# Performance work log

Hardware: AMD Instinct MI355X
Metric: run time of the kernel (lower is better)

The kernel has to match this reference:

```python
import jax, jax.numpy as jnp
import numpy as np

# Static problem sizes (see shape_source)
B, SX, SY = 256, 256, 70          # graphs, encoder nodes/graph, decoder nodes/graph
F, EMB, H = 512, 256, 256          # f_size, emb_size, h_size
VOCAB = 256
E = 4 * B * SY                     # 71680 edges
N_SLT = 4                          # SltEdgeTypes
N_SRT = 8                          # len(SrtEdgeTypes)


def setup_inputs() -> dict:
    key = jax.random.key(0)
    ks = jax.random.split(key, 24)
    s = 0.02
    inp = {
        'x': jax.random.normal(ks[0], (B * SX, F), jnp.float32),
        'x_batch': jnp.repeat(jnp.arange(B, dtype=jnp.int64), SX),
        'tgt_y': jax.random.randint(ks[1], (B * SY,), 0, VOCAB, jnp.int64),
        'tgt_edge_index': jax.random.randint(ks[2], (2, E), 0, B * SY, jnp.int64),
        'tgt_edge_type': jax.random.randint(ks[3], (E,), 0, N_SLT, jnp.int64),
        'tgt_y_batch': jnp.repeat(jnp.arange(B, dtype=jnp.int64), SY),
        'embeds': jax.random.normal(ks[4], (VOCAB, EMB), jnp.float32) * s,
    }
    dims = [(EMB, H), (H, H), (H, EMB)]
    k = 5
    for l, (din, dout) in enumerate(dims, start=1):
        inp[f'W_in{l}'] = jax.random.normal(ks[k + 0], (din, dout), jnp.float32) * s
        inp[f'Wq{l}'] = jax.random.normal(ks[k + 1], (dout, F), jnp.float32) * s
        inp[f'Wv{l}'] = jax.random.normal(ks[k + 2], (F, dout), jnp.float32) * s
        inp[f'Ee{l}'] = jax.random.normal(ks[k + 3], (N_SLT, dout), jnp.float32) * s
        k += 4
    inp['lin_z_w'] = jax.random.normal(ks[k], (EMB, VOCAB), jnp.float32) * s
    inp['lin_z_b'] = jnp.zeros((VOCAB,), jnp.float32)
    inp['lin_g_w'] = jax.random.normal(ks[k + 1], (2 * EMB, N_SRT), jnp.float32) * s
    inp['lin_g_b'] = jnp.zeros((N_SRT,), jnp.float32)
    return inp


def gcn_dec_layer(x_b, y, src, tgt, etype, W_in, Wq, Wv, Ee):
    """Edge-type-conditioned message passing + cross-attention onto encoder x.
    x_b: [B,SX,F]; y: [Ny,din]. Returns ([Ny,dout], alpha [B,SY,SX])."""
    h = y @ W_in                                   # [Ny, dout]
    m = h[src] + Ee[etype]                         # gather + type embedding
    agg = jax.ops.segment_sum(m, tgt, num_segments=y.shape[0])
    q = (h @ Wq).reshape(B, SY, F)                 # query into encoder space
    logits = jnp.einsum('bqf,bkf->bqk', q, x_b) / jnp.sqrt(jnp.float32(F))
    alpha = jax.nn.softmax(logits, axis=-1)        # [B,SY,SX]
    ctx = jnp.einsum('bqk,bkf->bqf', alpha, x_b) @ Wv  # [B,SY,dout]
    out = jax.nn.relu(h + agg + ctx.reshape(h.shape[0], -1))
    return out, alpha


def reference(x, x_batch, tgt_y, tgt_edge_index, tgt_edge_type, tgt_y_batch,
              embeds, W_in1, Wq1, Wv1, Ee1, W_in2, Wq2, Wv2, Ee2,
              W_in3, Wq3, Wv3, Ee3, lin_z_w, lin_z_b, lin_g_w, lin_g_b):
    x_b = x.reshape(B, SX, F)
    src, tgt = tgt_edge_index[0], tgt_edge_index[1]
    y = embeds[tgt_y]                              # [Ny, EMB]
    y, a1 = gcn_dec_layer(x_b, y, src, tgt, tgt_edge_type, W_in1, Wq1, Wv1, Ee1)
    y, a2 = gcn_dec_layer(x_b, y, src, tgt, tgt_edge_type, W_in2, Wq2, Wv2, Ee2)
    y, a3 = gcn_dec_layer(x_b, y, src, tgt, tgt_edge_type, W_in3, Wq3, Wv3, Ee3)
    y_score = y @ lin_z_w + lin_z_b                # [Ny, VOCAB]
    ef = y[tgt_edge_index]                         # [2, E, EMB]
    ef = jnp.transpose(ef, (1, 0, 2)).reshape(E, 2 * EMB)
    y_edge_rel_score = ef @ lin_g_w + lin_g_b      # [E, N_SRT]
    return (y, y_score, y_edge_rel_score, a1, a2, a3)
```

## Files before the change

### kernel.cpp

```cpp
#include <hip/hip_runtime.h>
#include <cstddef>
#include <cstdint>

#define B_    256
#define SX_   256
#define SY_   70
#define F_    512
#define EMB_  256
#define NY_   (B_*SY_)
#define NE_   (4*B_*SY_)

typedef short s16x8 __attribute__((ext_vector_type(8)));
typedef float f32x4 __attribute__((ext_vector_type(4)));
typedef unsigned short us4 __attribute__((ext_vector_type(4)));
typedef unsigned short us8 __attribute__((ext_vector_type(8)));

__device__ __forceinline__ unsigned short f2bf(float f) {
    unsigned u = __builtin_bit_cast(unsigned, f);
    u += 0x7fffu + ((u >> 16) & 1u);
    return (unsigned short)(u >> 16);
}
__device__ __forceinline__ float bf2f(unsigned short b) {
    unsigned u = ((unsigned)b) << 16;
    return __builtin_bit_cast(float, u);
}

template<int EPI>
__global__ __launch_bounds__(256, 2)
void gemm_mfma(const unsigned short* __restrict__ A, int lda, long sAb,
               const unsigned short* __restrict__ Bt, int ldb, long sBb,
               float* __restrict__ Cf, int ldc, long sCfb,
               unsigned short* __restrict__ Cb, int ldcb, long sCbb,
               const float* __restrict__ aux1, long sAux,
               int M, int K, float scale)
{
    __shared__ unsigned short As[128 * 64];
    __shared__ unsigned short Bs[128 * 64];
    char* AsB = (char*)As;
    char* BsB = (char*)Bs;
    const int tid = threadIdx.x;
    const int z = blockIdx.z;
    A  += (size_t)z * sAb;
    Bt += (size_t)z * sBb;
    if (aux1) aux1 += (size_t)z * sAux;
    const int bm = blockIdx.y * 128, bn = blockIdx.x * 128;
    const int lane = tid & 63;
    const int w = tid >> 6, wr = w >> 1, wc = w & 1;
    const int l15 = lane & 15, lq = lane >> 4;

    f32x4 acc[4][4];
    const f32x4 z4 = {0.f, 0.f, 0.f, 0.f};
#pragma unroll
    for (int m = 0; m < 4; ++m)
#pragma unroll
        for (int n = 0; n < 4; ++n) acc[m][n] = z4;

    for (int k0 = 0; k0 < K; k0 += 64) {
#pragma unroll
        for (int i = 0; i < 4; ++i) {
            const int row = i * 32 + (tid >> 3);
            const int k8  = (tid & 7) ^ (row & 7);
            int ra = bm + row; ra = (ra < M) ? ra : (M - 1);
            const unsigned short* g = A + (size_t)ra * lda + k0 + k8 * 8;
            __builtin_amdgcn_global_load_lds(
                (const __attribute__((address_space(1))) unsigned int*)g,
                (__attribute__((address_space(3))) unsigned int*)(AsB + i * 4096 + tid * 16),
                16, 0, 0);
        }
#pragma unroll
        for (int i = 0; i < 4; ++i) {
            const int row = i * 32 + (tid >> 3);
            const int k8  = (tid & 7) ^ (row & 7);
            const unsigned short* g = Bt + (size_t)(bn + row) * ldb + k0 + k8 * 8;
            __builtin_amdgcn_global_load_lds(
                (const __attribute__((address_space(1))) unsigned int*)g,
                (__attribute__((address_space(3))) unsigned int*)(BsB + i * 4096 + tid * 16),
                16, 0, 0);
        }
        __syncthreads();
#pragma unroll
        for (int kk = 0; kk < 2; ++kk) {
            s16x8 af[4], bf[4];
#pragma unroll
            for (int m = 0; m < 4; ++m) {
                const int row = wr * 64 + m * 16 + l15;
                const int slot = (kk * 4 + lq) ^ (row & 7);
                af[m] = *(const s16x8*)(AsB + row * 128 + slot * 16);
            }
#pragma unroll
            for (int n = 0; n < 4; ++n) {
                const int col = wc * 64 + n * 16 + l15;
                const int slot = (kk * 4 + lq) ^ (col & 7);
                bf[n] = *(const s16x8*)(BsB + col * 128 + slot * 16);
            }
#pragma unroll
            for (int m = 0; m < 4; ++m)
#pragma unroll
                for (int n = 0; n < 4; ++n)
                    acc[m][n] = __builtin_amdgcn_mfma_f32_16x16x32_bf16(
                        af[m], bf[n], acc[m][n], 0, 0, 0);
        }
        __syncthreads();
    }

    float* cf = Cf ? Cf + (size_t)z * sCfb : nullptr;
    unsigned short* cb = Cb ? Cb + (size_t)z * sCbb : nullptr;
#pragma unroll
    for (int m = 0; m < 4; ++m) {
#pragma unroll
        for (int n = 0; n < 4; ++n) {
            const int col = bn + wc * 64 + n * 16 + l15;
            f32x4 v = acc[m][n];
#pragma unroll
            for (int r = 0; r < 4; ++r) {
                const int gr = bm + wr * 64 + m * 16 + lq * 4 + r;
                if (gr >= M) continue;
                float o = v[r] * scale;
                if (EPI == 4) o += aux1[col];
                if (EPI == 5) {
                    o += aux1[(size_t)gr * ldc + col];
                    o = fmaxf(o, 0.f);
                }
                if (cf) cf[(size_t)gr * ldc + col] = o;
                if (cb) cb[(size_t)gr * ldcb + col] = f2bf(o);
            }
        }
    }
}

__global__ __launch_bounds__(256, 1)
void attn_logits_sm(const unsigned short* __restrict__ Q,
                    const unsigned short* __restrict__ X,
                    float* __restrict__ Aout,
                    unsigned short* __restrict__ Ab,
                    float scale)
{
    __shared__ unsigned short As[128 * 64];
    __shared__ unsigned short Bs[256 * 64];
    __shared__ float red[2][2][64];
    char* AsB = (char*)As;
    char* BsB = (char*)Bs;
    const int tid = threadIdx.x;
    const int z = blockIdx.x;
    const unsigned short* Qb = Q + (size_t)z * SY_ * F_;
    const unsigned short* Xb = X + (size_t)z * SX_ * F_;
    const int lane = tid & 63;
    const int w = tid >> 6, wr = w >> 1, wc = w & 1;
    const int l15 = lane & 15, lq = lane >> 4;

    f32x4 acc[4][8];
    const f32x4 z4 = {0.f, 0.f, 0.f, 0.f};
#pragma unroll
    for (int m = 0; m < 4; ++m)
#pragma unroll
        for (int n = 0; n < 8; ++n) acc[m][n] = z4;

    for (int k0 = 0; k0 < F_; k0 += 64) {
#pragma unroll
        for (int i = 0; i < 4; ++i) {
            const int row = i * 32 + (tid >> 3);
            const int k8  = (tid & 7) ^ (row & 7);
            const int ra = (row < SY_) ? row : (SY_ - 1);
            const unsigned short* g = Qb + (size_t)ra * F_ + k0 + k8 * 8;
            __builtin_amdgcn_global_load_lds(
                (const __attribute__((address_space(1))) unsigned int*)g,
                (__attribute__((address_space(3))) unsigned int*)(AsB + i * 4096 + tid * 16),
                16, 0, 0);
        }
#pragma unroll
        for (int i = 0; i < 8; ++i) {
            const int row = i * 32 + (tid >> 3);
            const int k8  = (tid & 7) ^ (row & 7);
            const unsigned short* g = Xb + (size_t)row * F_ + k0 + k8 * 8;
            __builtin_amdgcn_global_load_lds(
                (const __attribute__((address_space(1))) unsigned int*)g,
                (__attribute__((address_space(3))) unsigned int*)(BsB + i * 4096 + tid * 16),
                16, 0, 0);
        }
        __syncthreads();
#pragma unroll
        for (int kk = 0; kk < 2; ++kk) {
            s16x8 af[4], bf[8];
#pragma unroll
            for (int m = 0; m < 4; ++m) {
                const int row = wr * 64 + m * 16 + l15;
                const int slot = (kk * 4 + lq) ^ (row & 7);
                af[m] = *(const s16x8*)(AsB + row * 128 + slot * 16);
            }
#pragma unroll
            for (int n = 0; n < 8; ++n) {
                const int col = wc * 128 + n * 16 + l15;
                const int slot = (kk * 4 + lq) ^ (col & 7);
                bf[n] = *(const s16x8*)(BsB + col * 128 + slot * 16);
            }
#pragma unroll
            for (int m = 0; m < 4; ++m)
#pragma unroll
                for (int n = 0; n < 8; ++n)
                    acc[m][n] = __builtin_amdgcn_mfma_f32_16x16x32_bf16(
                        af[m], bf[n], acc[m][n], 0, 0, 0);
        }
        __syncthreads();
    }

#pragma unroll
    for (int m = 0; m < 4; ++m)
#pragma unroll
        for (int n = 0; n < 8; ++n)
#pragma unroll
            for (int r = 0; r < 4; ++r) acc[m][n][r] *= scale;

    float rmax[4][4];
#pragma unroll
    for (int m = 0; m < 4; ++m)
#pragma unroll
        for (int r = 0; r < 4; ++r) {
            float mx = acc[m][0][r];
#pragma unroll
            for (int n = 1; n < 8; ++n) mx = fmaxf(mx, acc[m][n][r]);
            mx = fmaxf(mx, __shfl_xor(mx, 1));
            mx = fmaxf(mx, __shfl_xor(mx, 2));
            mx = fmaxf(mx, __shfl_xor(mx, 4));
            mx = fmaxf(mx, __shfl_xor(mx, 8));
            rmax[m][r] = mx;
        }
    if (l15 == 0) {
#pragma unroll
        for (int m = 0; m < 4; ++m)
#pragma unroll
            for (int r = 0; r < 4; ++r)
                red[wc][wr][m * 16 + lq * 4 + r] = rmax[m][r];
    }
    __syncthreads();
    float rtot[4][4];
#pragma unroll
    for (int m = 0; m < 4; ++m)
#pragma unroll
        for (int r = 0; r < 4; ++r) {
            const int lr = m * 16 + lq * 4 + r;
            rtot[m][r] = fmaxf(red[0][wr][lr], red[1][wr][lr]);
        }
    __syncthreads();
    float rsum[4][4];
#pragma unroll
    for (int m = 0; m < 4; ++m)
#pragma unroll
        for (int r = 0; r < 4; ++r) {
            float s = 0.f;
#pragma unroll
            for (int n = 0; n < 8; ++n) {
                float e = __expf(acc[m][n][r] - rtot[m][r]);
                acc[m][n][r] = e;
                s += e;
            }
            s += __shfl_xor(s, 1);
            s += __shfl_xor(s, 2);
            s += __shfl_xor(s, 4);
            s += __shfl_xor(s, 8);
            rsum[m][r] = s;
        }
    if (l15 == 0) {
#pragma unroll
        for (int m = 0; m < 4; ++m)
#pragma unroll
            for (int r = 0; r < 4; ++r)
                red[wc][wr][m * 16 + lq * 4 + r] = rsum[m][r];
    }
    __syncthreads();
    float* ao = Aout + (size_t)z * SY_ * SX_;
    unsigned short* ab = Ab + (size_t)z * SY_ * SX_;
#pragma unroll
    for (int m = 0; m < 4; ++m)
#pragma unroll
        for (int r = 0; r < 4; ++r) {
            const int lr = m * 16 + lq * 4 + r;
            const int row = wr * 64 + lr;
            if (row >= SY_) continue;
            const float inv = 1.0f / (red[0][wr][lr] + red[1][wr][lr]);
#pragma unroll
            for (int n = 0; n < 8; ++n) {
                const int col = wc * 128 + n * 16 + l15;
                const float o = acc[m][n][r] * inv;
                ao[(size_t)row * SX_ + col] = o;
                ab[(size_t)row * SX_ + col] = f2bf(o);
            }
        }
}

__global__ __launch_bounds__(256)
void conv_x(const float* __restrict__ in, unsigned short* __restrict__ out, int n8)
{
    for (int i = blockIdx.x * 256 + threadIdx.x; i < n8; i += 2048 * 256) {
        float4 a = ((const float4*)in)[i * 2];
        float4 b = ((const float4*)in)[i * 2 + 1];
        us8 o = { f2bf(a.x), f2bf(a.y), f2bf(a.z), f2bf(a.w),
                  f2bf(b.x), f2bf(b.y), f2bf(b.z), f2bf(b.w) };
        ((us8*)out)[i] = o;
    }
}

struct WAll {
    const float* src[10];
    unsigned short* dst[10];
    int R[10];
    int C[10];
};

__global__ __launch_bounds__(256)
void conv_wT_all(WAll d)
{
    const int z = blockIdx.z;
    const int R = d.R[z], C = d.C[z];
    const int c0 = blockIdx.x * 64, r0 = blockIdx.y * 64;
    if (c0 >= C || r0 >= R) return;
    const float* in = d.src[z];
    unsigned short* outT = d.dst[z];
    __shared__ unsigned short t[64][65];
    const int r = threadIdx.x >> 4, cq = (threadIdx.x & 15) << 2;
#pragma unroll
    for (int i = 0; i < 4; ++i) {
        const int rr = r + i * 16;
        float4 v = *(const float4*)(in + (size_t)(r0 + rr) * C + c0 + cq);
        t[rr][cq + 0] = f2bf(v.x); t[rr][cq + 1] = f2bf(v.y);
        t[rr][cq + 2] = f2bf(v.z); t[rr][cq + 3] = f2bf(v.w);
    }
    __syncthreads();
    const int c = threadIdx.x >> 2, sq = (threadIdx.x & 3) << 4;
    us8 o0, o1;
#pragma unroll
    for (int i = 0; i < 8; ++i) { o0[i] = t[sq + i][c]; o1[i] = t[sq + 8 + i][c]; }
    *(us8*)(outT + (size_t)(c0 + c) * R + r0 + sq) = o0;
    *(us8*)(outT + (size_t)(c0 + c) * R + r0 + sq + 8) = o1;
}

__global__ __launch_bounds__(256)
void gather_embed(const float* __restrict__ embeds, const int* __restrict__ tgt_y,
                  unsigned short* __restrict__ yb)
{
    const int i = blockIdx.x * 8 + (threadIdx.x >> 5);
    const int c8 = (threadIdx.x & 31) * 8;
    const int v = tgt_y[i];
    const float* p = embeds + (size_t)v * 256 + c8;
    float4 a = *(const float4*)p;
    float4 b = *(const float4*)(p + 4);
    us8 o = { f2bf(a.x), f2bf(a.y), f2bf(a.z), f2bf(a.w),
              f2bf(b.x), f2bf(b.y), f2bf(b.z), f2bf(b.w) };
    *(us8*)(yb + (size_t)i * 256 + c8) = o;
}

__global__ __launch_bounds__(256)
void edge_deg(const int* __restrict__ tgt, int* __restrict__ deg)
{
    const int e = blockIdx.x * 256 + threadIdx.x;
    if (e < NE_) atomicAdd(&deg[tgt[e]], 1);
}

__global__ __launch_bounds__(1024)
void scan_off(const int* __restrict__ deg, int* __restrict__ off, int* __restrict__ cursor)
{
    __shared__ int ls[1024];
    const int t = threadIdx.x;
    const int base = t * 18;
    int local[18];
    int s = 0;
#pragma unroll
    for (int i = 0; i < 18; ++i) {
        const int idx = base + i;
        const int v = (idx < NY_) ? deg[idx] : 0;
        local[i] = s; s += v;
    }
    ls[t] = s;
    __syncthreads();
    for (int d = 1; d < 1024; d <<= 1) {
        int v = (t >= d) ? ls[t - d] : 0;
        __syncthreads();
        ls[t] += v;
        __syncthreads();
    }
    const int excl = (t == 0) ? 0 : ls[t - 1];
#pragma unroll
    for (int i = 0; i < 18; ++i) {
        const int idx = base + i;
        if (idx < NY_) {
            const int o = excl + local[i];
            off[idx] = o; cursor[idx] = o;
        }
    }
    if (t == 1023) off[NY_] = ls[1023];
}

__global__ __launch_bounds__(256)
void edge_fill(const int* __restrict__ tgt, int* __restrict__ cursor,
               int* __restrict__ elist)
{
    const int e = blockIdx.x * 256 + threadIdx.x;
    if (e >= NE_) return;
    const int pos = atomicAdd(&cursor[tgt[e]], 1);
    elist[pos] = e;
}

__global__ __launch_bounds__(256)
void node_agg(const unsigned short* __restrict__ hb,
              const float* __restrict__ Ee,
              const int* __restrict__ src, const int* __restrict__ etype,
              const int* __restrict__ off, const int* __restrict__ elist,
              float* __restrict__ agg)
{
    const int nid  = blockIdx.x * 4 + (threadIdx.x >> 6);
    const int lane = threadIdx.x & 63;
    const int c = lane * 4;
    const int k0 = off[nid], k1 = off[nid + 1];
    us4 sv = *(const us4*)(hb + (size_t)nid * 256 + c);
    float4 acc;
    acc.x = bf2f(sv[0]); acc.y = bf2f(sv[1]);
    acc.z = bf2f(sv[2]); acc.w = bf2f(sv[3]);
    int cnt0 = 0, cnt1 = 0, cnt2 = 0, cnt3 = 0;
    for (int k = k0; k < k1; ++k) {
        const int e = elist[k];
        const int sfrom = src[e];
        const int ty = etype[e];
        us4 hv = *(const us4*)(hb + (size_t)sfrom * 256 + c);
        acc.x += bf2f(hv[0]); acc.y += bf2f(hv[1]);
        acc.z += bf2f(hv[2]); acc.w += bf2f(hv[3]);
        cnt0 += (ty == 0); cnt1 += (ty == 1); cnt2 += (ty == 2); cnt3 += (ty == 3);
    }
    float4 e0 = *(const float4*)(Ee + c);
    float4 e1 = *(const float4*)(Ee + 256 + c);
    float4 e2 = *(const float4*)(Ee + 512 + c);
    float4 e3 = *(const float4*)(Ee + 768 + c);
    acc.x += cnt0 * e0.x + cnt1 * e1.x + cnt2 * e2.x + cnt3 * e3.x;
    acc.y += cnt0 * e0.y + cnt1 * e1.y + cnt2 * e2.y + cnt3 * e3.y;
    acc.z += cnt0 * e0.z + cnt1 * e1.z + cnt2 * e2.z + cnt3 * e3.z;
    acc.w += cnt0 * e0.w + cnt1 * e1.w + cnt2 * e2.w + cnt3 * e3.w;
    *(float4*)(agg + (size_t)nid * 256 + c) = acc;
}

__global__ __launch_bounds__(256)
void edge_w(const float* __restrict__ y, const float* __restrict__ W,
            float* __restrict__ Y12)
{
    __shared__ float Ws[4096];
    __shared__ float ys[16][260];
    const int tid = threadIdx.x;
#pragma unroll
    for (int i = 0; i < 4; ++i)
        ((float4*)Ws)[i * 256 + tid] = ((const float4*)W)[i * 256 + tid];
    const int r = tid >> 4, seg = tid & 15;
    const int r0 = blockIdx.x * 16;
#pragma unroll
    for (int i = 0; i < 4; ++i) {
        const int c4 = seg + i * 16;
        *(float4*)&ys[r][c4 * 4] = *(const float4*)(y + (size_t)(r0 + r) * 256 + c4 * 4);
    }
    __syncthreads();
    const int j = tid & 15;
    const int row = tid >> 4;
    const float* Wcol = Ws + ((j < 8) ? j : (2048 + j - 8));
    float acc = 0.f;
#pragma unroll 4
    for (int c = 0; c < 256; ++c) acc = fmaf(ys[row][c], Wcol[c * 8], acc);
    Y12[(size_t)(r0 + row) * 16 + j] = acc;
}

__global__ __launch_bounds__(256)
void edge_gather(const float* __restrict__ Y12, const int* __restrict__ src,
                 const int* __restrict__ tgt, const float* __restrict__ bias,
                 float* __restrict__ esc)
{
    const int e = blockIdx.x * 256 + threadIdx.x;
    if (e >= NE_) return;
    const float* a = Y12 + (size_t)src[e] * 16;
    const float* b = Y12 + (size_t)tgt[e] * 16 + 8;
    float4 a0 = ((const float4*)a)[0], a1 = ((const float4*)a)[1];
    float4 b0 = ((const float4*)b)[0], b1 = ((const float4*)b)[1];
    float4 c0 = ((const float4*)bias)[0], c1 = ((const float4*)bias)[1];
    float4 o0, o1;
    o0.x = a0.x + b0.x + c0.x; o0.y = a0.y + b0.y + c0.y;
    o0.z = a0.z + b0.z + c0.z; o0.w = a0.w + b0.w + c0.w;
    o1.x = a1.x + b1.x + c1.x; o1.y = a1.y + b1.y + c1.y;
    o1.z = a1.z + b1.z + c1.z; o1.w = a1.w + b1.w + c1.w;
    ((float4*)(esc + (size_t)e * 8))[0] = o0;
    ((float4*)(esc + (size_t)e * 8))[1] = o1;
}

extern "C" void kernel_launch(void* const* d_in, const int* in_sizes, int n_in,
                              void* d_out, int out_size, void* d_ws, size_t ws_size,
                              hipStream_t stream)
{
    const float* x       = (const float*)d_in[0];
    const int*   tgt_y   = (const int*)d_in[2];
    const int*   eidx    = (const int*)d_in[3];
    const int*   etype   = (const int*)d_in[4];
    const float* embeds  = (const float*)d_in[6];
    const float* W_in[3] = {(const float*)d_in[7],  (const float*)d_in[11], (const float*)d_in[15]};
    const float* Wq[3]   = {(const float*)d_in[8],  (const float*)d_in[12], (const float*)d_in[16]};
    const float* Wv[3]   = {(const float*)d_in[9],  (const float*)d_in[13], (const float*)d_in[17]};
    const float* Ee[3]   = {(const float*)d_in[10], (const float*)d_in[14], (const float*)d_in[18]};
    const float* lin_z_w = (const float*)d_in[19];
    const float* lin_z_b = (const float*)d_in[20];
    const float* lin_g_w = (const float*)d_in[21];
    const float* lin_g_b = (const float*)d_in[22];
    const int* src = eidx;
    const int* tgt = eidx + NE_;

    float* out = (float*)d_out;
    float* y_final = out;
    float* score   = out + 4587520;
    float* esc     = out + 9175040;
    float* aout[3] = {out + 9748480, out + 14336000, out + 18923520};

    char* wsb = (char*)d_ws;
    unsigned short* xb     = (unsigned short*)(wsb + 0);
    unsigned short* xvTall = (unsigned short*)(wsb + 67108864);
    unsigned short* hb     = (unsigned short*)(wsb + 167772160);
    float*          agg    = (float*)         (wsb + 176947200);
    unsigned short* qb     = (unsigned short*)(wsb + 195297280);
    unsigned short* yb     = (unsigned short*)(wsb + 213647360);
    char* wt = wsb + 222822400;
    unsigned short* winT[3], *wqT[3], *wvT[3];
    for (int l = 0; l < 3; ++l) {
        winT[l] = (unsigned short*)(wt + l * 131072);
        wqT[l]  = (unsigned short*)(wt + 393216  + l * 262144);
        wvT[l]  = (unsigned short*)(wt + 1179648 + l * 262144);
    }
    unsigned short* lzT = (unsigned short*)(wt + 1966080);
    char* extra = wsb + 224919552;
    float* Y12    = (float*)extra;
    int*   deg    = (int*)(extra + 1146880);
    int*   off    = (int*)(extra + 1218560);
    int*   cursor = (int*)(extra + 1290244);
    int*   elist  = (int*)(extra + 1361924);

    hipMemsetAsync(deg, 0, NY_ * sizeof(int), stream);
    edge_deg<<<280, 256, 0, stream>>>(tgt, deg);
    scan_off<<<1, 1024, 0, stream>>>(deg, off, cursor);
    edge_fill<<<280, 256, 0, stream>>>(tgt, cursor, elist);

    conv_x<<<2048, 256, 0, stream>>>(x, xb, 4194304);
    WAll wd;
    for (int l = 0; l < 3; ++l) {
        wd.src[l]     = W_in[l]; wd.dst[l]     = winT[l]; wd.R[l]     = 256; wd.C[l]     = 256;
        wd.src[3 + l] = Wq[l];   wd.dst[3 + l] = wqT[l];  wd.R[3 + l] = 256; wd.C[3 + l] = 512;
        wd.src[6 + l] = Wv[l];   wd.dst[6 + l] = wvT[l];  wd.R[6 + l] = 512; wd.C[6 + l] = 256;
    }
    wd.src[9] = lin_z_w; wd.dst[9] = lzT; wd.R[9] = 256; wd.C[9] = 256;
    conv_wT_all<<<dim3(8, 8, 10), 256, 0, stream>>>(wd);
    gather_embed<<<2240, 256, 0, stream>>>(embeds, tgt_y, yb);

    gemm_mfma<0><<<dim3(2, 6, B_), 256, 0, stream>>>(
        wvT[0], 512, 0,  xb, 512, (long)SX_ * F_,
        nullptr, 0, 0,  xvTall, 256, 768L * 256,
        nullptr, 0, 768, 512, 1.f);

    const float qscale = 0.044194173824159216f;
    for (int l = 0; l < 3; ++l) {
        gemm_mfma<0><<<dim3(2, 140, 1), 256, 0, stream>>>(
            yb, 256, 0,  winT[l], 256, 0,
            nullptr, 0, 0,   hb, 256, 0,
            nullptr, 0, NY_, 256, 1.f);
        node_agg<<<4480, 256, 0, stream>>>(hb, Ee[l], src, etype, off, elist, agg);
        gemm_mfma<0><<<dim3(4, 140, 1), 256, 0, stream>>>(
            hb, 256, 0,  wqT[l], 256, 0,
            nullptr, 0, 0,  qb, 512, 0,
            nullptr, 0, NY_, 256, 1.f);
        attn_logits_sm<<<256, 256, 0, stream>>>(qb, xb, aout[l], hb, qscale);
        gemm_mfma<5><<<dim3(2, 1, B_), 256, 0, stream>>>(
            hb, 256, (long)SY_ * SX_,  xvTall + (size_t)l * 65536, 256, 768L * 256,
            (l == 2) ? y_final : nullptr, 256, (long)SY_ * EMB_,
            yb, 256, (long)SY_ * EMB_,
            agg, (long)SY_ * EMB_, SY_, 256, 1.f);
    }
    gemm_mfma<4><<<dim3(2, 140, 1), 256, 0, stream>>>(
        yb, 256, 0,  lzT, 256, 0,
        score, 256, 0,  nullptr, 0, 0,
        lin_z_b, 0, NY_, 256, 1.f);
    edge_w<<<1120, 256, 0, stream>>>(y_final, lin_g_w, Y12);
    edge_gather<<<280, 256, 0, stream>>>(Y12, src, tgt, lin_g_b, esc);
}
```

Measured before the change: 509.9 us.

## Use 8 waves in attention-softmax kernel and XCD-swizzle batched Wv GEMM

The attention logits+softmax kernel now runs 512 threads per block, with each wave covering a 64-column slice instead of 128. This halves per-thread accumulator registers and adds latency hiding, and the row max/sum reduction now combines four column groups. The precomputed x@Wv GEMM is launched as a flat 1D grid with an XCD-aware block index remap, so adjacent tiles of the same batch land on the same chiplet and share L2. The cost is extra index arithmetic and more cross-wave shared-memory reduction.

```diff
diff --git a/kernel.cpp b/kernel.cpp
--- a/kernel.cpp
+++ b/kernel.cpp
@@ -25,25 +25,35 @@
     return __builtin_bit_cast(float, u);
 }
 
-template<int EPI>
+template<int EPI, int SWZ>
 __global__ __launch_bounds__(256, 2)
 void gemm_mfma(const unsigned short* __restrict__ A, int lda, long sAb,
                const unsigned short* __restrict__ Bt, int ldb, long sBb,
                float* __restrict__ Cf, int ldc, long sCfb,
                unsigned short* __restrict__ Cb, int ldcb, long sCbb,
                const float* __restrict__ aux1, long sAux,
-               int M, int K, float scale)
+               int M, int K, float scale, int nx, int ny)
 {
     __shared__ unsigned short As[128 * 64];
     __shared__ unsigned short Bs[128 * 64];
     char* AsB = (char*)As;
     char* BsB = (char*)Bs;
     const int tid = threadIdx.x;
-    const int z = blockIdx.z;
+    int bxi, byi, z;
+    if (SWZ) {
+        const int nwg = gridDim.x;
+        const int bid = blockIdx.x;
+        const int wg = (bid & 7) * (nwg >> 3) + (bid >> 3);
+        bxi = wg % nx;
+        byi = (wg / nx) % ny;
+        z   = wg / (nx * ny);
+    } else {
+        bxi = blockIdx.x; byi = blockIdx.y; z = blockIdx.z;
+    }
     A  += (size_t)z * sAb;
     Bt += (size_t)z * sBb;
     if (aux1) aux1 += (size_t)z * sAux;
-    const int bm = blockIdx.y * 128, bn = blockIdx.x * 128;
+    const int bm = byi * 128, bn = bxi * 128;
     const int lane = tid & 63;
     const int w = tid >> 6, wr = w >> 1, wc = w & 1;
     const int l15 = lane & 15, lq = lane >> 4;
@@ -128,7 +138,7 @@
     }
 }
 
-__global__ __launch_bounds__(256, 1)
+__global__ __launch_bounds__(512, 1)
 void attn_logits_sm(const unsigned short* __restrict__ Q,
                     const unsigned short* __restrict__ X,
                     float* __restrict__ Aout,
@@ -137,7 +147,7 @@
 {
     __shared__ unsigned short As[128 * 64];
     __shared__ unsigned short Bs[256 * 64];
-    __shared__ float red[2][2][64];
+    __shared__ float red[4][2][64];
     char* AsB = (char*)As;
     char* BsB = (char*)Bs;
     const int tid = threadIdx.x;
@@ -145,42 +155,42 @@
     const unsigned short* Qb = Q + (size_t)z * SY_ * F_;
     const unsigned short* Xb = X + (size_t)z * SX_ * F_;
     const int lane = tid & 63;
-    const int w = tid >> 6, wr = w >> 1, wc = w & 1;
+    const int w = tid >> 6, wr = w >> 2, wc = w & 3;
     const int l15 = lane & 15, lq = lane >> 4;
 
-    f32x4 acc[4][8];
+    f32x4 acc[4][4];
     const f32x4 z4 = {0.f, 0.f, 0.f, 0.f};
 #pragma unroll
     for (int m = 0; m < 4; ++m)
 #pragma unroll
-        for (int n = 0; n < 8; ++n) acc[m][n] = z4;
+        for (int n = 0; n < 4; ++n) acc[m][n] = z4;
 
     for (int k0 = 0; k0 < F_; k0 += 64) {
 #pragma unroll
-        for (int i = 0; i < 4; ++i) {
-            const int row = i * 32 + (tid >> 3);
+        for (int i = 0; i < 2; ++i) {
+            const int row = i * 64 + (tid >> 3);
             const int k8  = (tid & 7) ^ (row & 7);
             const int ra = (row < SY_) ? row : (SY_ - 1);
             const unsigned short* g = Qb + (size_t)ra * F_ + k0 + k8 * 8;
             __builtin_amdgcn_global_load_lds(
                 (const __attribute__((address_space(1))) unsigned int*)g,
-                (__attribute__((address_space(3))) unsigned int*)(AsB + i * 4096 + tid * 16),
+                (__attribute__((address_space(3))) unsigned int*)(AsB + i * 8192 + tid * 16),
                 16, 0, 0);
         }
 #pragma unroll
-        for (int i = 0; i < 8; ++i) {
-            const int row = i * 32 + (tid >> 3);
+        for (int i = 0; i < 4; ++i) {
+            const int row = i * 64 + (tid >> 3);
             const int k8  = (tid & 7) ^ (row & 7);
             const unsigned short* g = Xb + (size_t)row * F_ + k0 + k8 * 8;
             __builtin_amdgcn_global_load_lds(
                 (const __attribute__((address_space(1))) unsigned int*)g,
-                (__attribute__((address_space(3))) unsigned int*)(BsB + i * 4096 + tid * 16),
+                (__attribute__((address_space(3))) unsigned int*)(BsB + i * 8192 + tid * 16),
                 16, 0, 0);
         }
         __syncthreads();
 #pragma unroll
         for (int kk = 0; kk < 2; ++kk) {
-            s16x8 af[4], bf[8];
+            s16x8 af[4], bf[4];
 #pragma unroll
             for (int m = 0; m < 4; ++m) {
                 const int row = wr * 64 + m * 16 + l15;
@@ -188,15 +198,15 @@
                 af[m] = *(const s16x8*)(AsB + row * 128 + slot * 16);
             }
 #pragma unroll
-            for (int n = 0; n < 8; ++n) {
-                const int col = wc * 128 + n * 16 + l15;
+            for (int n = 0; n < 4; ++n) {
+                const int col = wc * 64 + n * 16 + l15;
                 const int slot = (kk * 4 + lq) ^ (col & 7);
                 bf[n] = *(const s16x8*)(BsB + col * 128 + slot * 16);
             }
 #pragma unroll
             for (int m = 0; m < 4; ++m)
 #pragma unroll
-                for (int n = 0; n < 8; ++n)
+                for (int n = 0; n < 4; ++n)
                     acc[m][n] = __builtin_amdgcn_mfma_f32_16x16x32_bf16(
                         af[m], bf[n], acc[m][n], 0, 0, 0);
         }
@@ -206,7 +216,7 @@
 #pragma unroll
     for (int m = 0; m < 4; ++m)
 #pragma unroll
-        for (int n = 0; n < 8; ++n)
+        for (int n = 0; n < 4; ++n)
 #pragma unroll
             for (int r = 0; r < 4; ++r) acc[m][n][r] *= scale;
 
@@ -217,7 +227,7 @@
         for (int r = 0; r < 4; ++r) {
             float mx = acc[m][0][r];
 #pragma unroll
-            for (int n = 1; n < 8; ++n) mx = fmaxf(mx, acc[m][n][r]);
+            for (int n = 1; n < 4; ++n) mx = fmaxf(mx, acc[m][n][r]);
             mx = fmaxf(mx, __shfl_xor(mx, 1));
             mx = fmaxf(mx, __shfl_xor(mx, 2));
             mx = fmaxf(mx, __shfl_xor(mx, 4));
@@ -238,7 +248,8 @@
 #pragma unroll
         for (int r = 0; r < 4; ++r) {
             const int lr = m * 16 + lq * 4 + r;
-            rtot[m][r] = fmaxf(red[0][wr][lr], red[1][wr][lr]);
+            rtot[m][r] = fmaxf(fmaxf(red[0][wr][lr], red[1][wr][lr]),
+                               fmaxf(red[2][wr][lr], red[3][wr][lr]));
         }
     __syncthreads();
     float rsum[4][4];
@@ -248,7 +259,7 @@
         for (int r = 0; r < 4; ++r) {
             float s = 0.f;
 #pragma unroll
-            for (int n = 0; n < 8; ++n) {
+            for (int n = 0; n < 4; ++n) {
                 float e = __expf(acc[m][n][r] - rtot[m][r]);
                 acc[m][n][r] = e;
                 s += e;
@@ -276,10 +287,11 @@
             const int lr = m * 16 + lq * 4 + r;
             const int row = wr * 64 + lr;
             if (row >= SY_) continue;
-            const float inv = 1.0f / (red[0][wr][lr] + red[1][wr][lr]);
-#pragma unroll
-            for (int n = 0; n < 8; ++n) {
-                const int col = wc * 128 + n * 16 + l15;
+            const float inv = 1.0f / (red[0][wr][lr] + red[1][wr][lr] +
+                                      red[2][wr][lr] + red[3][wr][lr]);
+#pragma unroll
+            for (int n = 0; n < 4; ++n) {
+                const int col = wc * 64 + n * 16 + l15;
                 const float o = acc[m][n][r] * inv;
                 ao[(size_t)row * SX_ + col] = o;
                 ab[(size_t)row * SX_ + col] = f2bf(o);
@@ -547,33 +559,33 @@
     conv_wT_all<<<dim3(8, 8, 10), 256, 0, stream>>>(wd);
     gather_embed<<<2240, 256, 0, stream>>>(embeds, tgt_y, yb);
 
-    gemm_mfma<0><<<dim3(2, 6, B_), 256, 0, stream>>>(
+    gemm_mfma<0, 1><<<3072, 256, 0, stream>>>(
         wvT[0], 512, 0,  xb, 512, (long)SX_ * F_,
         nullptr, 0, 0,  xvTall, 256, 768L * 256,
-        nullptr, 0, 768, 512, 1.f);
+        nullptr, 0, 768, 512, 1.f, 2, 6);
 
     const float qscale = 0.044194173824159216f;
     for (int l = 0; l < 3; ++l) {
-        gemm_mfma<0><<<dim3(2, 140, 1), 256, 0, stream>>>(
+        gemm_mfma<0, 0><<<dim3(2, 140, 1), 256, 0, stream>>>(
             yb, 256, 0,  winT[l], 256, 0,
             nullptr, 0, 0,   hb, 256, 0,
-            nullptr, 0, NY_, 256, 1.f);
+            nullptr, 0, NY_, 256, 1.f, 0, 0);
         node_agg<<<4480, 256, 0, stream>>>(hb, Ee[l], src, etype, off, elist, agg);
-        gemm_mfma<0><<<dim3(4, 140, 1), 256, 0, stream>>>(
+        gemm_mfma<0, 0><<<dim3(4, 140, 1), 256, 0, stream>>>(
             hb, 256, 0,  wqT[l], 256, 0,
             nullptr, 0, 0,  qb, 512, 0,
-            nullptr, 0, NY_, 256, 1.f);
-        attn_logits_sm<<<256, 256, 0, stream>>>(qb, xb, aout[l], hb, qscale);
-        gemm_mfma<5><<<dim3(2, 1, B_), 256, 0, stream>>>(
+            nullptr, 0, NY_, 256, 1.f, 0, 0);
+        attn_logits_sm<<<256, 512, 0, stream>>>(qb, xb, aout[l], hb, qscale);
+        gemm_mfma<5, 0><<<dim3(2, 1, B_), 256, 0, stream>>>(
             hb, 256, (long)SY_ * SX_,  xvTall + (size_t)l * 65536, 256, 768L * 256,
             (l == 2) ? y_final : nullptr, 256, (long)SY_ * EMB_,
             yb, 256, (long)SY_ * EMB_,
-            agg, (long)SY_ * EMB_, SY_, 256, 1.f);
-    }
-    gemm_mfma<4><<<dim3(2, 140, 1), 256, 0, stream>>>(
+            agg, (long)SY_ * EMB_, SY_, 256, 1.f, 0, 0);
+    }
+    gemm_mfma<4, 0><<<dim3(2, 140, 1), 256, 0, stream>>>(
         yb, 256, 0,  lzT, 256, 0,
         score, 256, 0,  nullptr, 0, 0,
-        lin_z_b, 0, NY_, 256, 1.f);
+        lin_z_b, 0, NY_, 256, 1.f, 0, 0);
     edge_w<<<1120, 256, 0, stream>>>(y_final, lin_g_w, Y12);
     edge_gather<<<280, 256, 0, stream>>>(Y12, src, tgt, lin_g_b, esc);
 }
```

New measurement: 493.3 us. 3.3% less time.
